# Performance work log

Measured on AMD Instinct MI355X. Metric: run time of the kernel, lower is better.

The kernel has to match this reference:

```python
import jax, jax.numpy as jnp
import numpy as np

N = 65536      # nodes
E = 1048576    # edges (avg degree 16)
B = 64         # graphs in batch
H = 128        # hidden
L = 3          # message-passing layers
MAXZ = 100


def _segment_mean(x, idx, n):
    s = jax.ops.segment_sum(x, idx, num_segments=n)
    c = jax.ops.segment_sum(jnp.ones((idx.shape[0], 1), x.dtype), idx, num_segments=n)
    return s / jnp.maximum(c, 1.0)


def setup_inputs() -> dict:
    key = jax.random.key(0)
    ks = jax.random.split(key, 24)
    w = lambda k, shape: jax.random.normal(k, shape, dtype=jnp.float32) * 0.05
    inp = {
        "pos": jax.random.normal(ks[0], (N, 3), dtype=jnp.float32),
        "z": jax.random.randint(ks[1], (N,), 0, MAXZ),
        "batch": jnp.sort(jax.random.randint(ks[2], (N,), 0, B)),
        "edge_index": jax.random.randint(ks[3], (2, E), 0, N),
        "node_type": jax.random.randint(ks[4], (N,), 0, 2),
        # parameters (weights stored [in, out] so y = x @ W + b)
        "emb": w(ks[5], (MAXZ, H)),
        "lin_in_w": w(ks[6], (H + 3, H)),
        "lin_in_b": jnp.zeros((H,), jnp.float32),
        "msg_w1": w(ks[7], (L, 2 * H + 1, H)),
        "msg_b1": jnp.zeros((L, H), jnp.float32),
        "msg_w2": w(ks[8], (L, H, H)),
        "msg_b2": jnp.zeros((L, H), jnp.float32),
        "upd_w": w(ks[9], (L, 2 * H, H)),
        "upd_b": jnp.zeros((L, H), jnp.float32),
        "ro_w1": w(ks[10], (H, H)),
        "ro_b1": jnp.zeros((H,), jnp.float32),
        "ro_w2": w(ks[11], (H, 1)),
        "ro_b2": jnp.zeros((1,), jnp.float32),
    }
    return inp


def reference(pos, z, batch, edge_index, node_type,
              emb, lin_in_w, lin_in_b,
              msg_w1, msg_b1, msg_w2, msg_b2,
              upd_w, upd_b, ro_w1, ro_b1, ro_w2, ro_b2):
    # centroid-centered positions per graph
    center = _segment_mean(pos, batch, B)           # [B,3]
    pos_rel = pos - center[batch]                   # [N,3]

    x = jnp.concatenate([emb[z], pos_rel], axis=-1) @ lin_in_w + lin_in_b  # [N,H]

    row, col = edge_index[0], edge_index[1]
    rel = pos_rel[col] - pos_rel[row]               # [E,3]
    dist = jnp.linalg.norm(rel, axis=-1, keepdims=True)  # [E,1]

    for l in range(L):
        m_in = jnp.concatenate([x[col], x[row], dist], axis=-1)      # [E,2H+1]
        h = jax.nn.relu(m_in @ msg_w1[l] + msg_b1[l])
        m_ij = jax.nn.relu(h @ msg_w2[l] + msg_b2[l])                # [E,H] (dropout=identity, eval)
        m_i = _segment_mean(m_ij, row, N)                            # [N,H]
        x = jax.nn.relu(jnp.concatenate([x, m_i], axis=-1) @ upd_w[l] + upd_b[l])

    lig_mask = (node_type == 1).astype(x.dtype)                      # [N]
    lig_counts = jnp.maximum(jax.ops.segment_sum(lig_mask, batch, num_segments=B), 1.0)
    g = jax.ops.segment_sum(x * lig_mask[:, None], batch, num_segments=B)  # [B,H]
    g = g / lig_counts[:, None]

    hg = jax.nn.relu(g @ ro_w1 + ro_b1)
    affinity = (hg @ ro_w2 + ro_b2).squeeze(-1)                      # [B]
    return affinity
```

## Files before the change

### kernel.cpp

```cpp
#include <hip/hip_runtime.h>
#include <hip/hip_bf16.h>
#include <hip/hip_fp16.h>
#include <math.h>

#define NN 65536
#define NE 1048576
#define NB 64
#define HD 128
#define NL 3

#define O_CSUM   0
#define O_CCNT   192
#define O_LCNT   256
#define O_GSUM   320
#define O_DEGI   8512
#define O_POSREL 74048
#define O_RC     270656
#define O_XHI    1319232
#define O_XLO    5513536
#define O_P      9707840
#define O_DIST   13902144
#define O_Q      18096448
#define O_C1H    22290752
#define O_EW     22291456
#define O_MSUM   26485056
#define O_W2T    34873664
#define O_W1TH   34898240
#define O_W1TL   34947392
#define O_WUTH   34996544
#define O_WUTL   35045696
#define O_CHK    35094848

typedef __attribute__((ext_vector_type(8))) short bf16x8;
typedef __attribute__((ext_vector_type(8))) _Float16 f16x8;
typedef __attribute__((ext_vector_type(8))) unsigned short u16x8;
typedef __attribute__((ext_vector_type(4))) float f32x4;

__device__ __forceinline__ void atomAdd(float* p, float v) { unsafeAtomicAdd(p, v); }

__device__ __forceinline__ unsigned short f2bf(float f) {
    union { __hip_bfloat16 h; unsigned short u; } cv;
    cv.h = __float2bfloat16(f);
    return cv.u;
}
__device__ __forceinline__ float bf2f(unsigned short u) {
    union { float f; unsigned v; } c; c.v = ((unsigned)u) << 16; return c.f;
}
__device__ __forceinline__ void split2(float v, unsigned short& h, unsigned short& l) {
    h = f2bf(v); l = f2bf(v - bf2f(h));
}
__device__ __forceinline__ unsigned short f2h(float f) {
    union { __half h; unsigned short u; } c; c.h = __float2half(f); return c.u;
}

__global__ __launch_bounds__(256) void stats_kernel(
    const float* __restrict__ pos, const int* __restrict__ batch,
    const int* __restrict__ ntype,
    float* __restrict__ csum, float* __restrict__ ccnt, float* __restrict__ lcnt)
{
    __shared__ float s[NB * 5];
    const int tid = threadIdx.x;
    for (int i = tid; i < NB * 5; i += 256) s[i] = 0.f;
    __syncthreads();
    const int n = blockIdx.x * 256 + tid;
    const int b = batch[n];
    atomicAdd(&s[b*5+0], pos[n*3+0]);
    atomicAdd(&s[b*5+1], pos[n*3+1]);
    atomicAdd(&s[b*5+2], pos[n*3+2]);
    atomicAdd(&s[b*5+3], 1.f);
    if (ntype[n] == 1) atomicAdd(&s[b*5+4], 1.f);
    __syncthreads();
    for (int i = tid; i < NB * 5; i += 256) {
        float v = s[i];
        if (v != 0.f) {
            int b2 = i / 5, f = i - b2*5;
            if (f < 3)       atomAdd(&csum[b2*3+f], v);
            else if (f == 3) atomAdd(&ccnt[b2], v);
            else             atomAdd(&lcnt[b2], v);
        }
    }
}

__global__ __launch_bounds__(256) void deg_kernel(const int* __restrict__ row, int* __restrict__ degi)
{
    const int e = blockIdx.x * 256 + threadIdx.x;
    atomicAdd(&degi[row[e]], 1);
}

__global__ __launch_bounds__(256) void scanA_kernel(const int* __restrict__ degi, int* __restrict__ chunkSum)
{
    __shared__ int red[4];
    const int t = threadIdx.x, b = blockIdx.x;
    int v = degi[b*256 + t];
    #pragma unroll
    for (int off = 32; off > 0; off >>= 1) v += __shfl_down(v, off, 64);
    if ((t & 63) == 0) red[t >> 6] = v;
    __syncthreads();
    if (t == 0) chunkSum[b] = red[0] + red[1] + red[2] + red[3];
}

__global__ __launch_bounds__(256) void scanB_kernel(int* __restrict__ chunkSum)
{
    __shared__ int s[256];
    const int t = threadIdx.x;
    const int v = chunkSum[t];
    s[t] = v;
    __syncthreads();
    #pragma unroll
    for (int off = 1; off < 256; off <<= 1) {
        int u = (t >= off) ? s[t - off] : 0;
        __syncthreads();
        s[t] += u;
        __syncthreads();
    }
    chunkSum[t] = s[t] - v;
}

__global__ __launch_bounds__(256) void scanC_kernel(const int* __restrict__ degi,
                                                    const int* __restrict__ chunkOff,
                                                    int* __restrict__ rowStart)
{
    __shared__ int s[256];
    const int t = threadIdx.x, b = blockIdx.x;
    const int v = degi[b*256 + t];
    s[t] = v;
    __syncthreads();
    #pragma unroll
    for (int off = 1; off < 256; off <<= 1) {
        int u = (t >= off) ? s[t - off] : 0;
        __syncthreads();
        s[t] += u;
        __syncthreads();
    }
    rowStart[b*256 + t] = chunkOff[b] + s[t] - v;
}

__global__ __launch_bounds__(256) void scatter_kernel(
    const int* __restrict__ row, const int* __restrict__ col,
    const int* __restrict__ rowStart, int* __restrict__ cnt,
    unsigned int* __restrict__ rcS,
    const float* __restrict__ posrel, float* __restrict__ distS)
{
    const int e = blockIdx.x * 256 + threadIdx.x;
    const int r = row[e], c = col[e];
    const float dx = posrel[c*3+0] - posrel[r*3+0];
    const float dy = posrel[c*3+1] - posrel[r*3+1];
    const float dz = posrel[c*3+2] - posrel[r*3+2];
    const int p = rowStart[r] + atomicAdd(&cnt[r], 1);
    rcS[p] = ((unsigned)r << 16) | (unsigned)c;
    distS[p] = sqrtf(dx*dx + dy*dy + dz*dz);
}

__global__ __launch_bounds__(256) void posrel_kernel(
    const float* __restrict__ pos, const int* __restrict__ batch,
    const float* __restrict__ csum, const float* __restrict__ ccnt,
    float* __restrict__ posrel)
{
    const int n = blockIdx.x * 256 + threadIdx.x;
    const int b = batch[n];
    const float inv = 1.f / fmaxf(ccnt[b], 1.f);
    posrel[n*3+0] = pos[n*3+0] - csum[b*3+0]*inv;
    posrel[n*3+1] = pos[n*3+1] - csum[b*3+1]*inv;
    posrel[n*3+2] = pos[n*3+2] - csum[b*3+2]*inv;
}

__global__ __launch_bounds__(256) void wprep_kernel(
    const float* __restrict__ mw1, const float* __restrict__ uw,
    const float* __restrict__ mw2,
    const float* __restrict__ lin_w, const float* __restrict__ lin_b,
    const float* __restrict__ emb,
    unsigned short* __restrict__ w1th, unsigned short* __restrict__ w1tl,
    unsigned short* __restrict__ wuth, unsigned short* __restrict__ wutl,
    unsigned short* __restrict__ w2t, unsigned short* __restrict__ c1h,
    float* __restrict__ EW)
{
    const int idx = blockIdx.x * 256 + threadIdx.x;
    {
        const int l = idx >> 15, rem = idx & 32767;
        const int w = rem & 7, t = rem >> 3;
        const int c = t & 255, kb = t >> 8;
        const int k = kb*8 + w;
        const int kk = (c < 128) ? k : (128 + k);
        const int cc = c & 127;
        const float v = mw1[l*257*128 + kk*128 + cc];
        unsigned short h, lo; split2(v, h, lo);
        w1th[idx] = h; w1tl[idx] = lo;
    }
    {
        const int l = idx >> 15, rem = idx & 32767;
        const int w = rem & 7, t = rem >> 3;
        const int c = t & 127, kb = t >> 7;
        const int k = kb*8 + w;
        const float v = uw[l*256*128 + k*128 + c];
        unsigned short h, lo; split2(v, h, lo);
        wuth[idx] = h; wutl[idx] = lo;
    }
    if (idx < 49152) {
        const int l = idx >> 14, rem = idx & 16383;
        const int blk = rem >> 3, win = rem & 7;
        const int n = blk >> 4, cs = blk & 15;
        const int c = cs ^ (n & 7);
        const int k = c*8 + win;
        w2t[idx] = f2h(mw2[(l << 14) + k*128 + n]);
    }
    if (idx < 384) {
        const int l = idx >> 7, c = idx & 127;
        c1h[idx] = f2h(mw1[l*257*128 + 256*128 + c]);
    }
    if (idx < 12800) {
        const int j = idx & 127, zz = idx >> 7;
        float acc = lin_b[j];
        for (int k = 0; k < 128; ++k)
            acc += emb[zz*128 + k] * lin_w[k*128 + j];
        EW[idx] = acc;
    }
}

__global__ __launch_bounds__(256) void lin_in_kernel(
    const float* __restrict__ EW, const float* __restrict__ posrel,
    const int* __restrict__ zidx, const float* __restrict__ lin_w,
    unsigned short* __restrict__ xhi, unsigned short* __restrict__ xlo)
{
    const int tid = threadIdx.x;
    const int node = blockIdx.x * 16 + (tid >> 4);
    const int j0 = (tid & 15) * 8;

    const int zz = zidx[node];
    const float px = posrel[node*3+0], py = posrel[node*3+1], pz = posrel[node*3+2];

    const float4 e0 = *(const float4*)&EW[zz*128 + j0];
    const float4 e1 = *(const float4*)&EW[zz*128 + j0 + 4];
    const float4 wx0 = *(const float4*)&lin_w[128*128 + j0];
    const float4 wx1 = *(const float4*)&lin_w[128*128 + j0 + 4];
    const float4 wy0 = *(const float4*)&lin_w[129*128 + j0];
    const float4 wy1 = *(const float4*)&lin_w[129*128 + j0 + 4];
    const float4 wz0 = *(const float4*)&lin_w[130*128 + j0];
    const float4 wz1 = *(const float4*)&lin_w[130*128 + j0 + 4];

    float o[8];
    o[0] = e0.x + px*wx0.x + py*wy0.x + pz*wz0.x;
    o[1] = e0.y + px*wx0.y + py*wy0.y + pz*wz0.y;
    o[2] = e0.z + px*wx0.z + py*wy0.z + pz*wz0.z;
    o[3] = e0.w + px*wx0.w + py*wy0.w + pz*wz0.w;
    o[4] = e1.x + px*wx1.x + py*wy1.x + pz*wz1.x;
    o[5] = e1.y + px*wx1.y + py*wy1.y + pz*wz1.y;
    o[6] = e1.z + px*wx1.z + py*wy1.z + pz*wz1.z;
    o[7] = e1.w + px*wx1.w + py*wy1.w + pz*wz1.w;

    ushort4 h0, l0, h1, l1;
    split2(o[0], h0.x, l0.x); split2(o[1], h0.y, l0.y);
    split2(o[2], h0.z, l0.z); split2(o[3], h0.w, l0.w);
    split2(o[4], h1.x, l1.x); split2(o[5], h1.y, l1.y);
    split2(o[6], h1.z, l1.z); split2(o[7], h1.w, l1.w);
    *(ushort4*)&xhi[node*HD + j0]     = h0;
    *(ushort4*)&xhi[node*HD + j0 + 4] = h1;
    *(ushort4*)&xlo[node*HD + j0]     = l0;
    *(ushort4*)&xlo[node*HD + j0 + 4] = l1;
}

__global__ __launch_bounds__(256) void pq_gemm(
    const unsigned short* __restrict__ xhi, const unsigned short* __restrict__ xlo,
    const unsigned short* __restrict__ w1th, const unsigned short* __restrict__ w1tl,
    unsigned short* __restrict__ Ph, unsigned short* __restrict__ Qh,
    float* __restrict__ msum, const float* __restrict__ b1)
{
    const int tid = threadIdx.x;
    const int l = tid & 63, w = tid >> 6;
    const int mr = l & 15, qd = l >> 4;
    const int n0 = blockIdx.x * 64;
    const int c0 = w * 64;

    {
        float4* mz = (float4*)&msum[(long)blockIdx.x * 8192];
        const float4 z4 = make_float4(0.f, 0.f, 0.f, 0.f);
        #pragma unroll
        for (int it = 0; it < 8; ++it) mz[tid + it*256] = z4;
    }

    f32x4 acc[4][4];
    #pragma unroll
    for (int mt = 0; mt < 4; ++mt)
        #pragma unroll
        for (int nt = 0; nt < 4; ++nt) acc[mt][nt] = (f32x4){0.f,0.f,0.f,0.f};

    #pragma unroll
    for (int ks = 0; ks < 4; ++ks) {
        const int kof = ks*32 + qd*8;
        const int kb  = ks*4 + qd;
        bf16x8 ah[4], al[4], bh[4], bl[4];
        #pragma unroll
        for (int mt = 0; mt < 4; ++mt) {
            const int node = n0 + mt*16 + mr;
            ah[mt] = *(const bf16x8*)&xhi[node*HD + kof];
            al[mt] = *(const bf16x8*)&xlo[node*HD + kof];
        }
        #pragma unroll
        for (int nt = 0; nt < 4; ++nt) {
            const int c = c0 + nt*16 + mr;
            bh[nt] = *(const bf16x8*)&w1th[(kb << 11) + (c << 3)];
            bl[nt] = *(const bf16x8*)&w1tl[(kb << 11) + (c << 3)];
        }
        #pragma unroll
        for (int mt = 0; mt < 4; ++mt)
            #pragma unroll
            for (int nt = 0; nt < 4; ++nt) {
                acc[mt][nt] = __builtin_amdgcn_mfma_f32_16x16x32_bf16(bh[nt], ah[mt], acc[mt][nt], 0,0,0);
                acc[mt][nt] = __builtin_amdgcn_mfma_f32_16x16x32_bf16(bl[nt], ah[mt], acc[mt][nt], 0,0,0);
                acc[mt][nt] = __builtin_amdgcn_mfma_f32_16x16x32_bf16(bh[nt], al[mt], acc[mt][nt], 0,0,0);
            }
    }

    unsigned short* __restrict__ dst = (w < 2) ? Ph : Qh;
    const int cbase = (w < 2) ? c0 : c0 - 128;
    #pragma unroll
    for (int mt = 0; mt < 4; ++mt) {
        const int node = n0 + mt*16 + mr;
        #pragma unroll
        for (int nt = 0; nt < 4; ++nt) {
            const int ccb = cbase + nt*16 + qd*4;
            float4 bb4 = make_float4(0.f, 0.f, 0.f, 0.f);
            if (w >= 2) bb4 = *(const float4*)&b1[ccb];
            ushort4 o4;
            o4.x = f2h(acc[mt][nt][0] + bb4.x);
            o4.y = f2h(acc[mt][nt][1] + bb4.y);
            o4.z = f2h(acc[mt][nt][2] + bb4.z);
            o4.w = f2h(acc[mt][nt][3] + bb4.w);
            *(ushort4*)&dst[(long)node*HD + ccb] = o4;
        }
    }
}

__global__ __launch_bounds__(256) void upd_gemm(
    unsigned short* __restrict__ xhi, unsigned short* __restrict__ xlo,
    const float* __restrict__ msum, const int* __restrict__ degi,
    const unsigned short* __restrict__ wuth, const unsigned short* __restrict__ wutl,
    const float* __restrict__ bias)
{
    const int tid = threadIdx.x;
    const int l = tid & 63, w = tid >> 6;
    const int mr = l & 15, qd = l >> 4;
    const int n0 = blockIdx.x * 64 + w*16;
    const int node = n0 + mr;
    const float inv = 1.f / fmaxf((float)degi[node], 1.f);

    f32x4 acc[8];
    #pragma unroll
    for (int nt = 0; nt < 8; ++nt) acc[nt] = (f32x4){0.f,0.f,0.f,0.f};

    #pragma unroll 1
    for (int ks = 0; ks < 8; ++ks) {
        const int kof = ks*32 + qd*8;
        const int kb  = ks*4 + qd;
        bf16x8 ah, al;
        if (ks < 4) {
            ah = *(const bf16x8*)&xhi[node*HD + kof];
            al = *(const bf16x8*)&xlo[node*HD + kof];
        } else {
            const int mk = kof - 128;
            const float4 v0 = *(const float4*)&msum[(long)node*HD + mk];
            const float4 v1 = *(const float4*)&msum[(long)node*HD + mk + 4];
            union { bf16x8 v; unsigned short u[8]; } hh, ll;
            float vv[8] = { v0.x*inv, v0.y*inv, v0.z*inv, v0.w*inv,
                            v1.x*inv, v1.y*inv, v1.z*inv, v1.w*inv };
            #pragma unroll
            for (int i = 0; i < 8; ++i) split2(vv[i], hh.u[i], ll.u[i]);
            ah = hh.v; al = ll.v;
        }
        #pragma unroll
        for (int nt = 0; nt < 8; ++nt) {
            const int c = nt*16 + mr;
            const bf16x8 bh = *(const bf16x8*)&wuth[(kb << 10) + (c << 3)];
            const bf16x8 bl = *(const bf16x8*)&wutl[(kb << 10) + (c << 3)];
            acc[nt] = __builtin_amdgcn_mfma_f32_16x16x32_bf16(bh, ah, acc[nt], 0,0,0);
            acc[nt] = __builtin_amdgcn_mfma_f32_16x16x32_bf16(bl, ah, acc[nt], 0,0,0);
            acc[nt] = __builtin_amdgcn_mfma_f32_16x16x32_bf16(bh, al, acc[nt], 0,0,0);
        }
    }

    #pragma unroll
    for (int nt = 0; nt < 8; ++nt) {
        const int cb = nt*16 + qd*4;
        const float4 bb4 = *(const float4*)&bias[cb];
        float o0 = fmaxf(acc[nt][0] + bb4.x, 0.f);
        float o1 = fmaxf(acc[nt][1] + bb4.y, 0.f);
        float o2 = fmaxf(acc[nt][2] + bb4.z, 0.f);
        float o3 = fmaxf(acc[nt][3] + bb4.w, 0.f);
        ushort4 h4, l4;
        split2(o0, h4.x, l4.x); split2(o1, h4.y, l4.y);
        split2(o2, h4.z, l4.z); split2(o3, h4.w, l4.w);
        *(ushort4*)&xhi[(long)node*HD + cb] = h4;
        *(ushort4*)&xlo[(long)node*HD + cb] = l4;
    }
}

__global__ __launch_bounds__(256) void edge_msg_kernel(
    const unsigned short* __restrict__ Ph, const unsigned short* __restrict__ Qh,
    const float* __restrict__ distS,
    const unsigned int* __restrict__ rcS,
    const unsigned short* __restrict__ c1h,
    const unsigned short* __restrict__ w2t,
    const float* __restrict__ b2,
    float* __restrict__ msum)
{
    __shared__ __align__(16) unsigned short w2s[16384];
    const int tid = threadIdx.x;

    {
        const uint4* __restrict__ src = (const uint4*)w2t;
        uint4* dst = (uint4*)w2s;
        #pragma unroll
        for (int i = 0; i < 8; ++i) dst[tid + i*256] = src[tid + i*256];
    }

    const long e0 = (long)blockIdx.x * 256;
    const int l  = tid & 63;
    const int w  = tid >> 6;
    const int mr = l & 15;
    const int qd = l >> 4;
    const long ebase = e0 + w*64;

    const int aoff = ((mr >> 2) << 4) + (mr & 3);
    int ecol[4], erow[4];
    #pragma unroll
    for (int m = 0; m < 4; ++m) {
        const unsigned rc = rcS[ebase + aoff + m*4];
        erow[m] = (int)(rc >> 16); ecol[m] = (int)(rc & 0xffffu);
    }

    u16x8 praw[4][4];
    #pragma unroll
    for (int m = 0; m < 4; ++m)
        #pragma unroll
        for (int kk = 0; kk < 4; ++kk)
            praw[m][kk] = *(const u16x8*)&Ph[(long)ecol[m]*HD + kk*32 + qd*8];

    float edist[4];
    #pragma unroll
    for (int m = 0; m < 4; ++m) edist[m] = distS[ebase + aoff + m*4];

    unsigned rcv[16];
    {
        const uint4* rc4 = (const uint4*)&rcS[ebase + qd*16];
        #pragma unroll
        for (int i = 0; i < 4; ++i) {
            const uint4 v = rc4[i];
            rcv[i*4+0] = (v.x >> 16) << 7; rcv[i*4+1] = (v.y >> 16) << 7;
            rcv[i*4+2] = (v.z >> 16) << 7; rcv[i*4+3] = (v.w >> 16) << 7;
        }
    }
    unsigned sameMask = 0;
    #pragma unroll
    for (int i = 1; i < 16; ++i) if (rcv[i] == rcv[i-1]) sameMask |= (1u << i);

    float b2v[8];
    #pragma unroll
    for (int t = 0; t < 8; ++t) b2v[t] = b2[t*16 + mr];

    f16x8 c8[4];
    #pragma unroll
    for (int kk = 0; kk < 4; ++kk) {
        union { u16x8 raw; f16x8 v; } cu;
        cu.raw = ((const u16x8*)c1h)[kk*4 + qd];
        c8[kk] = cu.v;
    }

    const f16x8 z8 = {};
    f16x8 afr[4][4];
    #pragma unroll
    for (int m = 0; m < 4; ++m) {
        union { u16x8 raw; f16x8 v; } qu[4];
        #pragma unroll
        for (int kk = 0; kk < 4; ++kk)
            qu[kk].raw = *(const u16x8*)&Qh[(long)erow[m]*HD + kk*32 + qd*8];
        const _Float16 d16 = (_Float16)edist[m];
        #pragma unroll
        for (int kk = 0; kk < 4; ++kk) {
            union { u16x8 raw; f16x8 v; } pu; pu.raw = praw[m][kk];
            f16x8 s = pu.v + qu[kk].v + d16 * c8[kk];
            afr[m][kk] = __builtin_elementwise_max(s, z8);
        }
    }

    __syncthreads();

    #pragma unroll 1
    for (int t = 0; t < 8; ++t) {
        f16x8 bfr[4];
        #pragma unroll
        for (int kk = 0; kk < 4; ++kk) {
            const int c = kk*4 + qd;
            const int blk = (t*16 + mr)*16 + (c ^ (mr & 7));
            union { u16x8 raw; f16x8 v; } bu;
            bu.raw = *(const u16x8*)&w2s[blk*8];
            bfr[kk] = bu.v;
        }
        const int colg = t*16 + mr;
        const float bb = b2v[t];

        f32x4 acc[4];
        #pragma unroll
        for (int m = 0; m < 4; ++m) acc[m] = (f32x4){0.f, 0.f, 0.f, 0.f};
        #pragma unroll
        for (int kk = 0; kk < 4; ++kk)
            #pragma unroll
            for (int m = 0; m < 4; ++m)
                acc[m] = __builtin_amdgcn_mfma_f32_16x16x32_f16(afr[m][kk], bfr[kk], acc[m], 0, 0, 0);

        float run = 0.f;
        #pragma unroll
        for (int i = 0; i < 16; ++i) {
            const float v = fmaxf(acc[i>>2][i&3] + bb, 0.f);
            run = (sameMask & (1u << i)) ? run + v : v;
            if (!(sameMask & (2u << i)))
                atomAdd(&msum[(long)(rcv[i] + colg)], run);
        }
    }
}

__global__ __launch_bounds__(256) void gsum_kernel(
    const unsigned short* __restrict__ xhi, const unsigned short* __restrict__ xlo,
    const int* __restrict__ batch,
    const int* __restrict__ ntype, float* __restrict__ gsum)
{
    const int tid = threadIdx.x;
    const int cg = tid & 31;
    const int ns = tid >> 5;
    const int n0 = blockIdx.x * 512 + ns * 64;

    int bprev = -1;
    float4 run = make_float4(0.f, 0.f, 0.f, 0.f);
    for (int i = 0; i < 64; ++i) {
        const int n = n0 + i;
        if (ntype[n] != 1) continue;
        const int b = batch[n];
        const ushort4 h  = *(const ushort4*)&xhi[(long)n*HD + cg*4];
        const ushort4 lo = *(const ushort4*)&xlo[(long)n*HD + cg*4];
        float4 v;
        v.x = bf2f(h.x) + bf2f(lo.x);
        v.y = bf2f(h.y) + bf2f(lo.y);
        v.z = bf2f(h.z) + bf2f(lo.z);
        v.w = bf2f(h.w) + bf2f(lo.w);
        if (b != bprev) {
            if (bprev >= 0) {
                float* dst = &gsum[bprev*HD + cg*4];
                atomAdd(dst+0, run.x); atomAdd(dst+1, run.y);
                atomAdd(dst+2, run.z); atomAdd(dst+3, run.w);
            }
            bprev = b; run = v;
        } else {
            run.x += v.x; run.y += v.y; run.z += v.z; run.w += v.w;
        }
    }
    if (bprev >= 0) {
        float* dst = &gsum[bprev*HD + cg*4];
        atomAdd(dst+0, run.x); atomAdd(dst+1, run.y);
        atomAdd(dst+2, run.z); atomAdd(dst+3, run.w);
    }
}

__global__ __launch_bounds__(128) void readout_kernel(
    const float* __restrict__ gsum, const float* __restrict__ lcnt,
    const float* __restrict__ w1, const float* __restrict__ b1,
    const float* __restrict__ w2, const float* __restrict__ b2,
    float* __restrict__ out)
{
    __shared__ float gs[HD];
    __shared__ float red[2];
    const int b = blockIdx.x, j = threadIdx.x;
    gs[j] = gsum[b*HD + j] / fmaxf(lcnt[b], 1.f);
    __syncthreads();
    float acc = b1[j];
    for (int k = 0; k < HD; ++k) acc += gs[k]*w1[k*HD + j];
    float hg = fmaxf(acc, 0.f) * w2[j];
    #pragma unroll
    for (int off = 32; off > 0; off >>= 1) hg += __shfl_down(hg, off, 64);
    if ((j & 63) == 0) red[j >> 6] = hg;
    __syncthreads();
    if (j == 0) out[b] = red[0] + red[1] + b2[0];
}

extern "C" void kernel_launch(void* const* d_in, const int* in_sizes, int n_in,
                              void* d_out, int out_size, void* d_ws, size_t ws_size,
                              hipStream_t stream)
{
    const float* pos   = (const float*)d_in[0];
    const int*   z     = (const int*)d_in[1];
    const int*   batch = (const int*)d_in[2];
    const int*   eidx  = (const int*)d_in[3];
    const int*   ntype = (const int*)d_in[4];
    const float* emb   = (const float*)d_in[5];
    const float* lin_w = (const float*)d_in[6];
    const float* lin_b = (const float*)d_in[7];
    const float* mw1   = (const float*)d_in[8];
    const float* mb1   = (const float*)d_in[9];
    const float* mw2   = (const float*)d_in[10];
    const float* mb2   = (const float*)d_in[11];
    const float* uw    = (const float*)d_in[12];
    const float* ub    = (const float*)d_in[13];
    const float* rw1   = (const float*)d_in[14];
    const float* rb1   = (const float*)d_in[15];
    const float* rw2   = (const float*)d_in[16];
    const float* rb2   = (const float*)d_in[17];

    const int* row = eidx;
    const int* col = eidx + NE;

    float* ws     = (float*)d_ws;
    float* csum   = ws + O_CSUM;
    float* ccnt   = ws + O_CCNT;
    float* lcnt   = ws + O_LCNT;
    float* gsum   = ws + O_GSUM;
    int*   degi   = (int*)(ws + O_DEGI);
    float* posrel = ws + O_POSREL;
    unsigned int* rcS = (unsigned int*)(ws + O_RC);
    unsigned short* xhi = (unsigned short*)(ws + O_XHI);
    unsigned short* xlo = (unsigned short*)(ws + O_XLO);
    unsigned short* Ph  = (unsigned short*)(ws + O_P);
    float* distS  = ws + O_DIST;
    unsigned short* Qh  = (unsigned short*)(ws + O_Q);
    unsigned short* c1h = (unsigned short*)(ws + O_C1H);
    float* EW     = ws + O_EW;
    float* msum   = ws + O_MSUM;
    unsigned short* w2t  = (unsigned short*)(ws + O_W2T);
    unsigned short* w1th = (unsigned short*)(ws + O_W1TH);
    unsigned short* w1tl = (unsigned short*)(ws + O_W1TL);
    unsigned short* wuth = (unsigned short*)(ws + O_WUTH);
    unsigned short* wutl = (unsigned short*)(ws + O_WUTL);
    int* chunkSum = (int*)(ws + O_CHK);
    int* rowStart = (int*)xhi;
    int* cnt      = (int*)xhi + NN;

    (void)hipMemsetAsync(ws, 0, (size_t)(O_DEGI + NN) * sizeof(float), stream);
    (void)hipMemsetAsync(cnt, 0, (size_t)NN * sizeof(int), stream);

    stats_kernel  <<<NN/256, 256, 0, stream>>>(pos, batch, ntype, csum, ccnt, lcnt);
    deg_kernel    <<<NE/256, 256, 0, stream>>>(row, degi);
    posrel_kernel <<<NN/256, 256, 0, stream>>>(pos, batch, csum, ccnt, posrel);
    scanA_kernel  <<<256, 256, 0, stream>>>(degi, chunkSum);
    scanB_kernel  <<<1, 256, 0, stream>>>(chunkSum);
    scanC_kernel  <<<256, 256, 0, stream>>>(degi, chunkSum, rowStart);
    scatter_kernel<<<NE/256, 256, 0, stream>>>(row, col, rowStart, cnt, rcS, posrel, distS);
    wprep_kernel  <<<384, 256, 0, stream>>>(mw1, uw, mw2, lin_w, lin_b, emb,
                                            w1th, w1tl, wuth, wutl, w2t, c1h, EW);

    lin_in_kernel<<<NN/16, 256, 0, stream>>>(EW, posrel, z, lin_w, xhi, xlo);

    for (int l = 0; l < NL; ++l) {
        pq_gemm<<<NN/64, 256, 0, stream>>>(xhi, xlo,
                                           w1th + (size_t)l*32768, w1tl + (size_t)l*32768,
                                           Ph, Qh, msum, mb1 + (size_t)l*HD);
        edge_msg_kernel<<<NE/256, 256, 0, stream>>>(Ph, Qh, distS, rcS,
                                                    c1h + (size_t)l*HD,
                                                    w2t + (size_t)l*16384, mb2 + l*HD, msum);
        upd_gemm<<<NN/64, 256, 0, stream>>>(xhi, xlo, msum, degi,
                                            wuth + (size_t)l*32768, wutl + (size_t)l*32768,
                                            ub + l*HD);
    }

    gsum_kernel   <<<NN/512, 256, 0, stream>>>(xhi, xlo, batch, ntype, gsum);
    readout_kernel<<<NB, 128, 0, stream>>>(gsum, lcnt, rw1, rb1, rw2, rb2, (float*)d_out);
}
```

Baseline: 772.6 us.

## Pack row/col and distance per edge and reduce messages in LDS per block

The scatter kernel now writes the packed row/col index and the edge distance together as a single 8-byte record per edge, so the edge message kernel fetches both with one load stream. Because edges are sorted by row, each block accumulates its messages into an LDS buffer covering up to 24 consecutive destination rows, then flushes them to the global message sum. Rows owned entirely by the block are written with plain stores; only boundary rows shared with neighbouring blocks, and any rows past the LDS capacity, use global atomics. This aims to cut global atomic traffic on the message sum, in exchange for LDS atomics, an extra barrier and flush loop, and a wider read of the row indices.

Result: slower. 920.4 us (+19.1%).

```diff
diff --git a/kernel.cpp b/kernel.cpp
--- a/kernel.cpp
+++ b/kernel.cpp
@@ -8,6 +8,7 @@
 #define NB 64
 #define HD 128
 #define NL 3
+#define LDSROWS 24
 
 #define O_CSUM   0
 #define O_CCNT   192
@@ -19,7 +20,7 @@
 #define O_XHI    1319232
 #define O_XLO    5513536
 #define O_P      9707840
-#define O_DIST   13902144
+#define O_RCD    13902144
 #define O_Q      18096448
 #define O_C1H    22290752
 #define O_EW     22291456
@@ -138,17 +139,17 @@
 __global__ __launch_bounds__(256) void scatter_kernel(
     const int* __restrict__ row, const int* __restrict__ col,
     const int* __restrict__ rowStart, int* __restrict__ cnt,
-    unsigned int* __restrict__ rcS,
-    const float* __restrict__ posrel, float* __restrict__ distS)
+    uint2* __restrict__ rcD,
+    const float* __restrict__ posrel)
 {
     const int e = blockIdx.x * 256 + threadIdx.x;
     const int r = row[e], c = col[e];
     const float dx = posrel[c*3+0] - posrel[r*3+0];
     const float dy = posrel[c*3+1] - posrel[r*3+1];
     const float dz = posrel[c*3+2] - posrel[r*3+2];
+    const float dist = sqrtf(dx*dx + dy*dy + dz*dz);
     const int p = rowStart[r] + atomicAdd(&cnt[r], 1);
-    rcS[p] = ((unsigned)r << 16) | (unsigned)c;
-    distS[p] = sqrtf(dx*dx + dy*dy + dz*dz);
+    rcD[p] = make_uint2(((unsigned)r << 16) | (unsigned)c, __float_as_uint(dist));
 }
 
 __global__ __launch_bounds__(256) void posrel_kernel(
@@ -395,14 +396,14 @@
 
 __global__ __launch_bounds__(256) void edge_msg_kernel(
     const unsigned short* __restrict__ Ph, const unsigned short* __restrict__ Qh,
-    const float* __restrict__ distS,
-    const unsigned int* __restrict__ rcS,
+    const uint2* __restrict__ rcD,
     const unsigned short* __restrict__ c1h,
     const unsigned short* __restrict__ w2t,
     const float* __restrict__ b2,
     float* __restrict__ msum)
 {
     __shared__ __align__(16) unsigned short w2s[16384];
+    __shared__ float rowbuf[LDSROWS * 132];
     const int tid = threadIdx.x;
 
     {
@@ -410,6 +411,7 @@
         uint4* dst = (uint4*)w2s;
         #pragma unroll
         for (int i = 0; i < 8; ++i) dst[tid + i*256] = src[tid + i*256];
+        for (int i = tid; i < LDSROWS*132; i += 256) rowbuf[i] = 0.f;
     }
 
     const long e0 = (long)blockIdx.x * 256;
@@ -419,12 +421,21 @@
     const int qd = l >> 4;
     const long ebase = e0 + w*64;
 
+    const unsigned rowLo = rcD[e0].x >> 16;
+    const unsigned rowHi = rcD[e0 + 255].x >> 16;
+    const bool loShared = (blockIdx.x > 0) && ((rcD[e0 - 1].x >> 16) == rowLo);
+    const bool hiShared = (blockIdx.x < (NE/256 - 1)) && ((rcD[e0 + 256].x >> 16) == rowHi);
+    const int  nRows    = (int)(rowHi - rowLo) + 1;
+    const unsigned rowLo128 = rowLo << 7;
+
     const int aoff = ((mr >> 2) << 4) + (mr & 3);
     int ecol[4], erow[4];
+    float edist[4];
     #pragma unroll
     for (int m = 0; m < 4; ++m) {
-        const unsigned rc = rcS[ebase + aoff + m*4];
-        erow[m] = (int)(rc >> 16); ecol[m] = (int)(rc & 0xffffu);
+        const uint2 rd = rcD[ebase + aoff + m*4];
+        erow[m] = (int)(rd.x >> 16); ecol[m] = (int)(rd.x & 0xffffu);
+        edist[m] = __uint_as_float(rd.y);
     }
 
     u16x8 praw[4][4];
@@ -434,18 +445,14 @@
         for (int kk = 0; kk < 4; ++kk)
             praw[m][kk] = *(const u16x8*)&Ph[(long)ecol[m]*HD + kk*32 + qd*8];
 
-    float edist[4];
-    #pragma unroll
-    for (int m = 0; m < 4; ++m) edist[m] = distS[ebase + aoff + m*4];
-
     unsigned rcv[16];
     {
-        const uint4* rc4 = (const uint4*)&rcS[ebase + qd*16];
-        #pragma unroll
-        for (int i = 0; i < 4; ++i) {
+        const uint4* rc4 = (const uint4*)&rcD[ebase + qd*16];
+        #pragma unroll
+        for (int i = 0; i < 8; ++i) {
             const uint4 v = rc4[i];
-            rcv[i*4+0] = (v.x >> 16) << 7; rcv[i*4+1] = (v.y >> 16) << 7;
-            rcv[i*4+2] = (v.z >> 16) << 7; rcv[i*4+3] = (v.w >> 16) << 7;
+            rcv[i*2+0] = (v.x >> 16) << 7;
+            rcv[i*2+1] = (v.z >> 16) << 7;
         }
     }
     unsigned sameMask = 0;
@@ -511,9 +518,26 @@
         for (int i = 0; i < 16; ++i) {
             const float v = fmaxf(acc[i>>2][i&3] + bb, 0.f);
             run = (sameMask & (1u << i)) ? run + v : v;
-            if (!(sameMask & (2u << i)))
-                atomAdd(&msum[(long)(rcv[i] + colg)], run);
-        }
+            if (!(sameMask & (2u << i))) {
+                const unsigned rel = (rcv[i] - rowLo128) >> 7;
+                if (rel < (unsigned)LDSROWS)
+                    atomicAdd(&rowbuf[rel*132 + colg], run);
+                else
+                    atomAdd(&msum[(long)(rcv[i] + colg)], run);
+            }
+        }
+    }
+
+    __syncthreads();
+    const int fRows = (nRows < LDSROWS) ? nRows : LDSROWS;
+    for (int i = tid; i < fRows*128; i += 256) {
+        const int r = i >> 7, c = i & 127;
+        const float v = rowbuf[r*132 + c];
+        float* dst = &msum[(((long)rowLo + r) << 7) + c];
+        if ((r == 0 && loShared) || (r == nRows-1 && hiShared))
+            atomAdd(dst, v);
+        else
+            *dst = v;
     }
 }
 
@@ -612,11 +636,10 @@
     float* gsum   = ws + O_GSUM;
     int*   degi   = (int*)(ws + O_DEGI);
     float* posrel = ws + O_POSREL;
-    unsigned int* rcS = (unsigned int*)(ws + O_RC);
     unsigned short* xhi = (unsigned short*)(ws + O_XHI);
     unsigned short* xlo = (unsigned short*)(ws + O_XLO);
     unsigned short* Ph  = (unsigned short*)(ws + O_P);
-    float* distS  = ws + O_DIST;
+    uint2* rcD    = (uint2*)(ws + O_RCD);
     unsigned short* Qh  = (unsigned short*)(ws + O_Q);
     unsigned short* c1h = (unsigned short*)(ws + O_C1H);
     float* EW     = ws + O_EW;
@@ -639,7 +662,7 @@
     scanA_kernel  <<<256, 256, 0, stream>>>(degi, chunkSum);
     scanB_kernel  <<<1, 256, 0, stream>>>(chunkSum);
     scanC_kernel  <<<256, 256, 0, stream>>>(degi, chunkSum, rowStart);
-    scatter_kernel<<<NE/256, 256, 0, stream>>>(row, col, rowStart, cnt, rcS, posrel, distS);
+    scatter_kernel<<<NE/256, 256, 0, stream>>>(row, col, rowStart, cnt, rcD, posrel);
     wprep_kernel  <<<384, 256, 0, stream>>>(mw1, uw, mw2, lin_w, lin_b, emb,
                                             w1th, w1tl, wuth, wutl, w2t, c1h, EW);
 
@@ -649,7 +672,7 @@
         pq_gemm<<<NN/64, 256, 0, stream>>>(xhi, xlo,
                                            w1th + (size_t)l*32768, w1tl + (size_t)l*32768,
                                            Ph, Qh, msum, mb1 + (size_t)l*HD);
-        edge_msg_kernel<<<NE/256, 256, 0, stream>>>(Ph, Qh, distS, rcS,
+        edge_msg_kernel<<<NE/256, 256, 0, stream>>>(Ph, Qh, rcD,
                                                     c1h + (size_t)l*HD,
                                                     w2t + (size_t)l*16384, mb2 + l*HD, msum);
         upd_gemm<<<NN/64, 256, 0, stream>>>(xhi, xlo, msum, degi,
```
